# Kernel tuning notes

Hardware: AMD Instinct MI355X
Metric: run time of the kernel (lower is better)

The kernel has to match this reference:

```python
import jax, jax.numpy as jnp
import numpy as np

# Kernel codes matching style 'L;O2;P2;Y2,1,1;R0.5;W1,1'
KERNEL_CODES = ['L', 'O', 'P', 'Y', 'R', 'W']
SM_TEMP = 1.0


def _norm_sq(q, k):
    # q: [n,l,h,e], k: [n,s,h,e] -> [n,h,l,s]
    q2 = jnp.einsum('nlhe,nlhe->nhl', q, q)[..., None]        # [n,h,l,1]
    k2 = jnp.einsum('nshe,nshe->nhs', k, k)[:, :, None, :]     # [n,h,1,s]
    qk = jnp.einsum('nlhe,nshe->nhls', q, k)
    return q2 + k2 - 2.0 * qk


def _kernel(code, q, k):
    if code == 'L':
        return jnp.einsum('nlhe,nshe->nhls', q, k)
    if code == 'O':  # -log(1 + ns^(p/2)), p=2
        return -jnp.log1p(_norm_sq(q, k))
    if code == 'P':  # -(ns)^(p/2), p=2
        return -_norm_sq(q, k)
    if code == 'Y':  # (alpha*<q,k> + c)^p, p=2, alpha=1, c=1
        d = jnp.einsum('nlhe,nshe->nhls', q, k)
        return (d + 1.0) ** 2
    if code == 'R':  # exp(-gamma*ns), gamma=0.5
        return jnp.exp(-0.5 * _norm_sq(q, k))
    if code == 'W':  # cos(ns/a)*exp(-ns/b), a=b=1
        ns = _norm_sq(q, k)
        return jnp.cos(ns) * jnp.exp(-ns)
    raise ValueError(code)


def setup_inputs() -> dict:
    key = jax.random.key(0)
    k1, k2, k3, k4 = jax.random.split(key, 4)
    N, L, S, H, E, K = 2, 1024, 1024, 8, 64, 6
    return {
        'query': jax.random.normal(k1, (N, L, H, E), dtype=jnp.float32),
        'key': jax.random.normal(k2, (N, S, H, E), dtype=jnp.float32),
        'attn_mask_add': jnp.zeros((N, L, S), dtype=jnp.float32),
        'key_lengths_add': jnp.zeros((N, S), dtype=jnp.float32),
        'M': jax.random.uniform(k3, (H, E, K), dtype=jnp.float32),
        'C': jax.random.uniform(k4, (K, H, E, E), dtype=jnp.float32),
    }


def reference(query, key, attn_mask_add, key_lengths_add, M, C):
    # mixture weights pi: [n,l,h,k]
    pi = jax.nn.softmax(jnp.einsum('nlhe,hek->nlhk', query, M), axis=-1)
    out = None
    for c, code in enumerate(KERNEL_CODES):
        # htilde = tanh(query @ C[c]): [n,l,h,e]
        htilde = jnp.tanh(jnp.einsum('nlhe,hef->nlhf', query, C[c]))
        qk = _kernel(code, htilde, key)                    # [n,h,l,s]
        qk = qk + attn_mask_add[:, None] + key_lengths_add[:, None, None, :]
        sm = jax.nn.softmax(SM_TEMP * qk, axis=-1)
        w = jnp.transpose(pi[..., c], (0, 2, 1))[..., None]  # [n,h,l,1]
        term = sm * w
        out = term if out is None else out + term
    return out
```

## Files before the change

kernel.cpp:

```cpp
#include <hip/hip_runtime.h>
#include <hip/hip_bf16.h>
#include <math.h>

#define N_  2
#define H_  8
#define G_  16
#define L_  1024
#define S_  1024
#define E_  64
#define NC_ 6

typedef __attribute__((ext_vector_type(4))) float floatx4;
typedef __attribute__((ext_vector_type(8))) short short8;

#define MFMA16 __builtin_amdgcn_mfma_f32_16x16x32_bf16

#define AHAT_OFF   0
#define AHAT_BYTES (NC_*G_*L_*128*2)
#define KHAT_OFF   (AHAT_OFF + AHAT_BYTES)
#define KHAT_BYTES (G_*S_*128*2)
#define PI_OFF     (KHAT_OFF + KHAT_BYTES)
#define PI_BYTES   (NC_*G_*L_*4)
#define HSQ_OFF    (PI_OFF + PI_BYTES)
#define HSQ_BYTES  (NC_*G_*L_*4)
#define KSQ_OFF    (HSQ_OFF + HSQ_BYTES)
#define KSQ_BYTES  (G_*S_*4)

__device__ __forceinline__ float ftanh(float x) {
  return 1.0f - 2.0f * __builtin_amdgcn_rcpf(__expf(2.0f*x) + 1.0f);
}

__global__ __launch_bounds__(256) void k_htilde(
    const float* __restrict__ q, const float* __restrict__ C,
    __hip_bfloat16* __restrict__ Ahat, float* __restrict__ hsq) {
  extern __shared__ char smraw[];
  float* qs = (float*)smraw;
  float* Cs = qs + 128*68;

  const int lch = blockIdx.x, c = blockIdx.y, g = blockIdx.z;
  const int n = g >> 3, h = g & 7;
  const int l0 = lch * 128;
  const int t = threadIdx.x;

  for (int u = t; u < 2048; u += 256) {
    int row = u >> 4, seg = u & 15;
    *(float4*)(qs + row*68 + seg*4) =
      *(const float4*)(q + (((size_t)(n*L_ + l0 + row))*H_ + h)*E_ + seg*4);
  }
  for (int u = t; u < 1024; u += 256) {
    int e = u >> 4, seg = u & 15;
    *(float4*)(Cs + e*68 + seg*4) =
      *(const float4*)(C + (((size_t)(c*8 + h))*64 + e)*64 + seg*4);
  }
  __syncthreads();

  const int rg = t >> 3, fg = t & 7;
  float acc[4][8];
  #pragma unroll
  for (int i = 0; i < 4; i++)
    #pragma unroll
    for (int j = 0; j < 8; j++) acc[i][j] = 0.0f;

  #pragma unroll 4
  for (int e0 = 0; e0 < 64; e0 += 4) {
    float4 q4[4];
    #pragma unroll
    for (int i = 0; i < 4; i++)
      q4[i] = *(const float4*)(qs + (rg*4 + i)*68 + e0);
    #pragma unroll
    for (int ee = 0; ee < 4; ee++) {
      float4 ca = *(const float4*)(Cs + (e0+ee)*68 + fg*8);
      float4 cb = *(const float4*)(Cs + (e0+ee)*68 + fg*8 + 4);
      float c8[8] = {ca.x, ca.y, ca.z, ca.w, cb.x, cb.y, cb.z, cb.w};
      #pragma unroll
      for (int i = 0; i < 4; i++) {
        float qv = (ee == 0) ? q4[i].x : (ee == 1) ? q4[i].y
                 : (ee == 2) ? q4[i].z : q4[i].w;
        #pragma unroll
        for (int j = 0; j < 8; j++) acc[i][j] = fmaf(qv, c8[j], acc[i][j]);
      }
    }
  }

  #pragma unroll
  for (int i = 0; i < 4; i++) {
    int l = l0 + rg*4 + i;
    size_t rowb = (((size_t)(c*G_ + g))*L_ + l) * 128;
    float ss = 0.0f;
    short8 hi8, lo8;
    #pragma unroll
    for (int j = 0; j < 8; j++) {
      float hv = ftanh(acc[i][j]);
      ss += hv*hv;
      __hip_bfloat16 hi = __float2bfloat16(hv);
      __hip_bfloat16 lo = __float2bfloat16(hv - __bfloat162float(hi));
      short hs, ls;
      __builtin_memcpy(&hs, &hi, 2);
      __builtin_memcpy(&ls, &lo, 2);
      hi8[j] = hs; lo8[j] = ls;
    }
    *(short8*)((char*)Ahat + (rowb + fg*8)*2)      = hi8;
    *(short8*)((char*)Ahat + (rowb + 64 + fg*8)*2) = lo8;
    ss += __shfl_xor(ss, 1); ss += __shfl_xor(ss, 2); ss += __shfl_xor(ss, 4);
    if (fg == 0) hsq[((size_t)(c*G_ + g))*L_ + l] = ss;
  }
}

__global__ __launch_bounds__(256) void k_pi(
    const float* __restrict__ q, const float* __restrict__ M,
    float* __restrict__ pi_t) {
  __shared__ float Ms[384];
  const int g = blockIdx.x >> 2, lch = blockIdx.x & 3;
  const int n = g >> 3, h = g & 7;
  const int t = threadIdx.x;
  const int l = lch*256 + t;
  for (int u = t; u < 384; u += 256) Ms[u] = M[h*384 + u];
  __syncthreads();
  const float* qrow = q + (((size_t)(n*L_ + l))*H_ + h)*E_;
  float p[6] = {0.f, 0.f, 0.f, 0.f, 0.f, 0.f};
  #pragma unroll 8
  for (int e = 0; e < 64; e++) {
    float qv = qrow[e];
    #pragma unroll
    for (int k = 0; k < 6; k++) p[k] = fmaf(qv, Ms[e*6 + k], p[k]);
  }
  float mx = p[0];
  #pragma unroll
  for (int k = 1; k < 6; k++) mx = fmaxf(mx, p[k]);
  float den = 0.f;
  #pragma unroll
  for (int k = 0; k < 6; k++) den += __expf(p[k] - mx);
  float rden = __builtin_amdgcn_rcpf(den);
  #pragma unroll
  for (int k = 0; k < 6; k++)
    pi_t[((size_t)(k*G_ + g))*L_ + l] = __expf(p[k] - mx) * rden;
}

__global__ __launch_bounds__(256) void k_key(
    const float* __restrict__ key, __hip_bfloat16* __restrict__ Khat,
    float* __restrict__ ksq) {
  int t = threadIdx.x; int wv = t >> 6; int lane = t & 63;
  int r = blockIdx.x*4 + wv;
  int g = r >> 10; int s = r & 1023; int n = g >> 3; int h = g & 7;
  float v = key[(((size_t)(n*S_ + s))*H_ + h)*E_ + lane];
  __hip_bfloat16 hi = __float2bfloat16(v);
  __hip_bfloat16 lo = __float2bfloat16(v - __bfloat162float(hi));
  size_t base = ((size_t)g*S_ + s)*128;
  Khat[base + lane]      = hi;
  Khat[base + 64 + lane] = lo;
  float sq = v*v;
  #pragma unroll
  for (int off = 32; off; off >>= 1) sq += __shfl_xor(sq, off);
  if (lane == 0) ksq[(size_t)g*S_ + s] = sq;
}

#define LDS_K     0
#define LDS_KSQ   17408
#define LDS_KLEN  17664
#define LDS_ZRED  24576
#define LDS_MRED  26112
#define LDS_CST   27648
#define LDS_HSQ   28416
#define LDS_PI    28800
#define LDS_TOTAL 29184

__global__ __launch_bounds__(256, 2) void k_main(
    const __hip_bfloat16* __restrict__ Ahat, const __hip_bfloat16* __restrict__ Khat,
    const float* __restrict__ hsq, const float* __restrict__ ksq,
    const float* __restrict__ mask, const float* __restrict__ klen,
    const float* __restrict__ pi_t, float* __restrict__ out) {
  extern __shared__ char smraw[];
  char*   A6     = smraw;
  char*   K_lds  = smraw + LDS_K;
  float*  ksq_t  = (float*)(smraw + LDS_KSQ);
  float*  klen_t = (float*)(smraw + LDS_KLEN);
  float*  zred   = (float*)(smraw + LDS_ZRED);
  float*  mred   = (float*)(smraw + LDS_MRED);
  float2* cst    = (float2*)(smraw + LDS_CST);
  float*  hsq_s  = (float*)(smraw + LDS_HSQ);
  float*  pi_s   = (float*)(smraw + LDS_PI);

  const int l0 = blockIdx.x * 16; const int g = blockIdx.y; const int n = g >> 3;
  const int t = threadIdx.x; const int w = t >> 6; const int lane = t & 63;
  const int quad = lane >> 4; const int lc = lane & 15;

  #pragma unroll
  for (int rep = 0; rep < 6; rep++) {
    int u = t + rep*256; int cc = u >> 8; int rem = u & 255;
    int row = rem >> 4; int seg = rem & 15;
    *(int4*)(A6 + cc*4096 + row*256 + seg*16) =
      *(const int4*)((const char*)Ahat + (((size_t)(cc*G_+g))*L_ + l0 + row)*256 + seg*16);
  }
  if (t < 96) {
    size_t idx = ((size_t)((t >> 4)*G_ + g))*L_ + l0 + (t & 15);
    hsq_s[t] = hsq[idx];
    pi_s[t]  = pi_t[idx];
  }
  __syncthreads();

  short8 a6f[6][4];
  #pragma unroll
  for (int cc = 0; cc < 6; cc++)
    #pragma unroll
    for (int kt = 0; kt < 4; kt++)
      a6f[cc][kt] = *(const short8*)(A6 + cc*4096 + lc*256 + kt*64 + quad*16);

  float h1p[4], nh2[4], h4h[4], nh5[4];
  #pragma unroll
  for (int i = 0; i < 4; i++) {
    int r = quad*4 + i;
    h1p[i] = 1.0f + hsq_s[1*16 + r];
    nh2[i] = 64.0f - hsq_s[2*16 + r];
    h4h[i] = -0.5f * hsq_s[4*16 + r];
    nh5[i] = -hsq_s[5*16 + r];
  }

  float Zc[4][4], zp[4], m3[4], z3[4];
  #pragma unroll
  for (int i = 0; i < 4; i++) {
    #pragma unroll
    for (int c = 0; c < 4; c++) Zc[c][i] = 0.0f;
    zp[i] = 0.0f; m3[i] = -INFINITY; z3[i] = 0.0f;
  }

  #pragma unroll 1
  for (int st = 0; st < 16; st++) {
    int s0 = st*64;
    __syncthreads();
    #pragma unroll
    for (int rep = 0; rep < 4; rep++) {
      int u = t + rep*256; int row = u >> 4, seg = u & 15;
      *(int4*)(K_lds + row*272 + seg*16) =
        *(const int4*)((const char*)Khat + (((size_t)g)*S_ + s0 + row)*256 + seg*16);
    }
    if (t < 64) { ksq_t[t] = ksq[(size_t)g*S_ + s0 + t]; klen_t[t] = klen[(size_t)n*S_ + s0 + t]; }
    int scol = s0 + w*16 + lc;
    float mk[4];
    #pragma unroll
    for (int i = 0; i < 4; i++)
      mk[i] = mask[((size_t)(n*L_ + l0 + quad*4 + i))*S_ + scol];
    __syncthreads();
    short8 bfr[4];
    #pragma unroll
    for (int kt = 0; kt < 4; kt++)
      bfr[kt] = *(const short8*)(K_lds + (w*16 + lc)*272 + kt*64 + quad*16);
    float kq  = ksq_t[w*16 + lc];
    float klv = klen_t[w*16 + lc];
    float mv[4], Ev[4], oc[4], pc[4], rc[4], wc[4];
    #pragma unroll
    for (int i = 0; i < 4; i++) {
      mv[i] = mk[i] + klv;
      Ev[i] = __expf(mv[i]);
      oc[i] = h1p[i] + kq;
      pc[i] = nh2[i] - kq + mv[i];
      rc[i] = fmaf(-0.5f, kq, h4h[i]);
      wc[i] = nh5[i] - kq;
    }
    #pragma unroll
    for (int c = 0; c < 6; c++) {
      floatx4 a = {0.f, 0.f, 0.f, 0.f};
      a = MFMA16(a6f[c][0], bfr[0], a, 0,0,0);
      a = MFMA16(a6f[c][1], bfr[1], a, 0,0,0);
      a = MFMA16(a6f[c][0], bfr[2], a, 0,0,0);
      a = MFMA16(a6f[c][1], bfr[3], a, 0,0,0);
      a = MFMA16(a6f[c][2], bfr[0], a, 0,0,0);
      a = MFMA16(a6f[c][3], bfr[1], a, 0,0,0);
      #pragma unroll
      for (int i = 0; i < 4; i++) {
        float d = a[i];
        if (c == 0) {
          Zc[0][i] = fmaf(Ev[i], __expf(d), Zc[0][i]);
        } else if (c == 1) {
          Zc[1][i] = fmaf(Ev[i], __builtin_amdgcn_rcpf(fmaf(-2.f, d, oc[i])), Zc[1][i]);
        } else if (c == 2) {
          zp[i] += __expf(fmaf(2.f, d, pc[i]));
        } else if (c == 3) {
          float tt = d + 1.f;
          float x  = fmaf(tt, tt, mv[i]);
          float mn = fmaxf(m3[i], x);
          float e  = __expf(fminf(m3[i], x) - mn);
          z3[i] = (x > m3[i]) ? fmaf(z3[i], e, 1.0f) : (z3[i] + e);
          m3[i] = mn;
        } else if (c == 4) {
          Zc[2][i] = fmaf(Ev[i], __expf(__expf(d + rc[i])), Zc[2][i]);
        } else {
          float a5 = fmaf(2.f, d, wc[i]);
          Zc[3][i] = fmaf(Ev[i], __expf(__cosf(a5) * __expf(a5)), Zc[3][i]);
        }
      }
    }
  }

  #pragma unroll
  for (int off = 1; off < 16; off <<= 1) {
    #pragma unroll
    for (int c = 0; c < 4; c++)
      #pragma unroll
      for (int i = 0; i < 4; i++) Zc[c][i] += __shfl_xor(Zc[c][i], off);
    #pragma unroll
    for (int i = 0; i < 4; i++) {
      zp[i] += __shfl_xor(zp[i], off);
      float mo = __shfl_xor(m3[i], off);
      float zo = __shfl_xor(z3[i], off);
      float mn = fmaxf(m3[i], mo);
      float e  = __expf(fminf(m3[i], mo) - mn);
      z3[i] = (mo > m3[i]) ? fmaf(z3[i], e, zo) : fmaf(zo, e, z3[i]);
      m3[i] = mn;
    }
  }
  if (lc == 0) {
    static const int cmap[4] = {0, 1, 4, 5};
    #pragma unroll
    for (int c = 0; c < 4; c++)
      #pragma unroll
      for (int i = 0; i < 4; i++) {
        zred[w*96 + cmap[c]*16 + quad*4 + i] = Zc[c][i];
        mred[w*96 + cmap[c]*16 + quad*4 + i] = 0.f;
      }
    #pragma unroll
    for (int i = 0; i < 4; i++) {
      zred[w*96 + 2*16 + quad*4 + i] = zp[i];
      mred[w*96 + 2*16 + quad*4 + i] = 0.f;
      zred[w*96 + 3*16 + quad*4 + i] = z3[i];
      mred[w*96 + 3*16 + quad*4 + i] = m3[i];
    }
  }
  __syncthreads();
  if (t < 96) {
    int c = t >> 4;
    float z = zred[t], m = mred[t];
    if (c == 3) {
      #pragma unroll
      for (int w2 = 1; w2 < 4; w2++) {
        float mo = mred[w2*96 + t], zo = zred[w2*96 + t];
        float mn = fmaxf(m, mo);
        float e  = __expf(fminf(m, mo) - mn);
        z = (mo > m) ? fmaf(z, e, zo) : fmaf(zo, e, z);
        m = mn;
      }
    } else {
      #pragma unroll
      for (int w2 = 1; w2 < 4; w2++) z += zred[w2*96 + t];
    }
    cst[t] = make_float2(pi_s[t] / z, m);
  }
  __syncthreads();

  float ac[6][4], m3f[4];
  #pragma unroll
  for (int c = 0; c < 6; c++)
    #pragma unroll
    for (int i = 0; i < 4; i++) {
      float2 v = cst[c*16 + quad*4 + i];
      ac[c][i] = v.x;
      if (c == 3) m3f[i] = v.y;
    }

  #pragma unroll 1
  for (int st = 0; st < 16; st++) {
    int s0 = st*64;
    __syncthreads();
    #pragma unroll
    for (int rep = 0; rep < 4; rep++) {
      int u = t + rep*256; int row = u >> 4, seg = u & 15;
      *(int4*)(K_lds + row*272 + seg*16) =
        *(const int4*)((const char*)Khat + (((size_t)g)*S_ + s0 + row)*256 + seg*16);
    }
    if (t < 64) { ksq_t[t] = ksq[(size_t)g*S_ + s0 + t]; klen_t[t] = klen[(size_t)n*S_ + s0 + t]; }
    int scol = s0 + w*16 + lc;
    float mk[4];
    #pragma unroll
    for (int i = 0; i < 4; i++)
      mk[i] = mask[((size_t)(n*L_ + l0 + quad*4 + i))*S_ + scol];
    __syncthreads();
    short8 bfr[4];
    #pragma unroll
    for (int kt = 0; kt < 4; kt++)
      bfr[kt] = *(const short8*)(K_lds + (w*16 + lc)*272 + kt*64 + quad*16);
    float kq  = ksq_t[w*16 + lc];
    float klv = klen_t[w*16 + lc];
    float mv[4], Ev[4], oc[4], pc[4], rc[4], wc[4];
    #pragma unroll
    for (int i = 0; i < 4; i++) {
      mv[i] = mk[i] + klv;
      Ev[i] = __expf(mv[i]);
      oc[i] = h1p[i] + kq;
      pc[i] = nh2[i] - kq + mv[i];
      rc[i] = fmaf(-0.5f, kq, h4h[i]);
      wc[i] = nh5[i] - kq;
    }
    float Sacc[4] = {0.f, 0.f, 0.f, 0.f};
    float G[4]    = {0.f, 0.f, 0.f, 0.f};
    #pragma unroll
    for (int c = 0; c < 6; c++) {
      floatx4 a = {0.f, 0.f, 0.f, 0.f};
      a = MFMA16(a6f[c][0], bfr[0], a, 0,0,0);
      a = MFMA16(a6f[c][1], bfr[1], a, 0,0,0);
      a = MFMA16(a6f[c][0], bfr[2], a, 0,0,0);
      a = MFMA16(a6f[c][1], bfr[3], a, 0,0,0);
      a = MFMA16(a6f[c][2], bfr[0], a, 0,0,0);
      a = MFMA16(a6f[c][3], bfr[1], a, 0,0,0);
      #pragma unroll
      for (int i = 0; i < 4; i++) {
        float d = a[i];
        if (c == 0) {
          Sacc[i] = fmaf(ac[0][i], __expf(d), Sacc[i]);
        } else if (c == 1) {
          Sacc[i] = fmaf(ac[1][i], __builtin_amdgcn_rcpf(fmaf(-2.f, d, oc[i])), Sacc[i]);
        } else if (c == 2) {
          G[i] = fmaf(ac[2][i], __expf(fmaf(2.f, d, pc[i])), G[i]);
        } else if (c == 3) {
          float tt = d + 1.f;
          float x  = fmaf(tt, tt, mv[i]);
          G[i] = fmaf(ac[3][i], __expf(x - m3f[i]), G[i]);
        } else if (c == 4) {
          Sacc[i] = fmaf(ac[4][i], __expf(__expf(d + rc[i])), Sacc[i]);
        } else {
          float a5 = fmaf(2.f, d, wc[i]);
          Sacc[i] = fmaf(ac[5][i], __expf(__cosf(a5) * __expf(a5)), Sacc[i]);
        }
      }
    }
    #pragma unroll
    for (int i = 0; i < 4; i++)
      out[(((size_t)g)*L_ + l0 + quad*4 + i)*S_ + scol] = fmaf(Ev[i], Sacc[i], G[i]);
  }
}

extern "C" void kernel_launch(void* const* d_in, const int* in_sizes, int n_in,
                              void* d_out, int out_size, void* d_ws, size_t ws_size,
                              hipStream_t stream) {
  (void)in_sizes; (void)n_in; (void)out_size; (void)ws_size;
  const float* q    = (const float*)d_in[0];
  const float* key  = (const float*)d_in[1];
  const float* mask = (const float*)d_in[2];
  const float* klen = (const float*)d_in[3];
  const float* M    = (const float*)d_in[4];
  const float* C    = (const float*)d_in[5];
  char* ws = (char*)d_ws;
  __hip_bfloat16* Ahat = (__hip_bfloat16*)(ws + AHAT_OFF);
  __hip_bfloat16* Khat = (__hip_bfloat16*)(ws + KHAT_OFF);
  float* pi_t    = (float*)(ws + PI_OFF);
  float* hsq     = (float*)(ws + HSQ_OFF);
  float* ksq     = (float*)(ws + KSQ_OFF);
  float* out = (float*)d_out;

  k_htilde<<<dim3(8, 6, 16), 256, 52224, stream>>>(q, C, Ahat, hsq);
  k_key<<<4096, 256, 0, stream>>>(key, Khat, ksq);
  k_pi<<<64, 256, 0, stream>>>(q, M, pi_t);
  k_main<<<dim3(64, 16), 256, LDS_TOTAL, stream>>>(Ahat, Khat, hsq, ksq, mask, klen,
                                                   pi_t, out);
}
```

Baseline: 224.5 us.

## Load MFMA operands directly from global memory, dropping LDS staging and barriers

The kernel no longer stages the A6 query fragments, the K tiles, ksq, klen, hsq and pi through LDS. Each lane now reads its MFMA operand fragments and per-column scalars straight from global memory, which removes both per-iteration __syncthreads in the two S loops and shrinks LDS to the reduction buffers only. The aim is to cut barrier stalls and LDS traffic and to allow more resident blocks. The cost is that each wave reads its own K slice as strided 16-byte global loads, relying on L1/L2 for reuse, and that latency is exposed without prefetching.

```diff
diff --git a/kernel.cpp b/kernel.cpp
--- a/kernel.cpp
+++ b/kernel.cpp
@@ -154,15 +154,10 @@
   if (lane == 0) ksq[(size_t)g*S_ + s] = sq;
 }
 
-#define LDS_K     0
-#define LDS_KSQ   17408
-#define LDS_KLEN  17664
-#define LDS_ZRED  24576
-#define LDS_MRED  26112
-#define LDS_CST   27648
-#define LDS_HSQ   28416
-#define LDS_PI    28800
-#define LDS_TOTAL 29184
+#define LDS_ZRED  0
+#define LDS_MRED  1536
+#define LDS_CST   3072
+#define LDS_TOTAL 3840
 
 __global__ __launch_bounds__(256, 2) void k_main(
     const __hip_bfloat16* __restrict__ Ahat, const __hip_bfloat16* __restrict__ Khat,
@@ -170,49 +165,30 @@
     const float* __restrict__ mask, const float* __restrict__ klen,
     const float* __restrict__ pi_t, float* __restrict__ out) {
   extern __shared__ char smraw[];
-  char*   A6     = smraw;
-  char*   K_lds  = smraw + LDS_K;
-  float*  ksq_t  = (float*)(smraw + LDS_KSQ);
-  float*  klen_t = (float*)(smraw + LDS_KLEN);
   float*  zred   = (float*)(smraw + LDS_ZRED);
   float*  mred   = (float*)(smraw + LDS_MRED);
   float2* cst    = (float2*)(smraw + LDS_CST);
-  float*  hsq_s  = (float*)(smraw + LDS_HSQ);
-  float*  pi_s   = (float*)(smraw + LDS_PI);
 
   const int l0 = blockIdx.x * 16; const int g = blockIdx.y; const int n = g >> 3;
   const int t = threadIdx.x; const int w = t >> 6; const int lane = t & 63;
   const int quad = lane >> 4; const int lc = lane & 15;
 
-  #pragma unroll
-  for (int rep = 0; rep < 6; rep++) {
-    int u = t + rep*256; int cc = u >> 8; int rem = u & 255;
-    int row = rem >> 4; int seg = rem & 15;
-    *(int4*)(A6 + cc*4096 + row*256 + seg*16) =
-      *(const int4*)((const char*)Ahat + (((size_t)(cc*G_+g))*L_ + l0 + row)*256 + seg*16);
-  }
-  if (t < 96) {
-    size_t idx = ((size_t)((t >> 4)*G_ + g))*L_ + l0 + (t & 15);
-    hsq_s[t] = hsq[idx];
-    pi_s[t]  = pi_t[idx];
-  }
-  __syncthreads();
-
   short8 a6f[6][4];
   #pragma unroll
   for (int cc = 0; cc < 6; cc++)
     #pragma unroll
     for (int kt = 0; kt < 4; kt++)
-      a6f[cc][kt] = *(const short8*)(A6 + cc*4096 + lc*256 + kt*64 + quad*16);
+      a6f[cc][kt] = *(const short8*)((const char*)Ahat +
+          (((size_t)(cc*G_ + g))*L_ + l0 + lc)*256 + kt*64 + quad*16);
 
   float h1p[4], nh2[4], h4h[4], nh5[4];
   #pragma unroll
   for (int i = 0; i < 4; i++) {
     int r = quad*4 + i;
-    h1p[i] = 1.0f + hsq_s[1*16 + r];
-    nh2[i] = 64.0f - hsq_s[2*16 + r];
-    h4h[i] = -0.5f * hsq_s[4*16 + r];
-    nh5[i] = -hsq_s[5*16 + r];
+    h1p[i] = 1.0f + hsq[((size_t)(1*G_ + g))*L_ + l0 + r];
+    nh2[i] = 64.0f - hsq[((size_t)(2*G_ + g))*L_ + l0 + r];
+    h4h[i] = -0.5f * hsq[((size_t)(4*G_ + g))*L_ + l0 + r];
+    nh5[i] = -hsq[((size_t)(5*G_ + g))*L_ + l0 + r];
   }
 
   float Zc[4][4], zp[4], m3[4], z3[4];
@@ -226,26 +202,18 @@
   #pragma unroll 1
   for (int st = 0; st < 16; st++) {
     int s0 = st*64;
-    __syncthreads();
-    #pragma unroll
-    for (int rep = 0; rep < 4; rep++) {
-      int u = t + rep*256; int row = u >> 4, seg = u & 15;
-      *(int4*)(K_lds + row*272 + seg*16) =
-        *(const int4*)((const char*)Khat + (((size_t)g)*S_ + s0 + row)*256 + seg*16);
-    }
-    if (t < 64) { ksq_t[t] = ksq[(size_t)g*S_ + s0 + t]; klen_t[t] = klen[(size_t)n*S_ + s0 + t]; }
     int scol = s0 + w*16 + lc;
+    short8 bfr[4];
+    #pragma unroll
+    for (int kt = 0; kt < 4; kt++)
+      bfr[kt] = *(const short8*)((const char*)Khat +
+          (((size_t)g)*S_ + scol)*256 + kt*64 + quad*16);
+    float kq  = ksq[(size_t)g*S_ + scol];
+    float klv = klen[(size_t)n*S_ + scol];
     float mk[4];
     #pragma unroll
     for (int i = 0; i < 4; i++)
       mk[i] = mask[((size_t)(n*L_ + l0 + quad*4 + i))*S_ + scol];
-    __syncthreads();
-    short8 bfr[4];
-    #pragma unroll
-    for (int kt = 0; kt < 4; kt++)
-      bfr[kt] = *(const short8*)(K_lds + (w*16 + lc)*272 + kt*64 + quad*16);
-    float kq  = ksq_t[w*16 + lc];
-    float klv = klen_t[w*16 + lc];
     float mv[4], Ev[4], oc[4], pc[4], rc[4], wc[4];
     #pragma unroll
     for (int i = 0; i < 4; i++) {
@@ -342,7 +310,8 @@
       #pragma unroll
       for (int w2 = 1; w2 < 4; w2++) z += zred[w2*96 + t];
     }
-    cst[t] = make_float2(pi_s[t] / z, m);
+    float piv = pi_t[((size_t)((t >> 4)*G_ + g))*L_ + l0 + (t & 15)];
+    cst[t] = make_float2(piv / z, m);
   }
   __syncthreads();
 
@@ -359,26 +328,18 @@
   #pragma unroll 1
   for (int st = 0; st < 16; st++) {
     int s0 = st*64;
-    __syncthreads();
-    #pragma unroll
-    for (int rep = 0; rep < 4; rep++) {
-      int u = t + rep*256; int row = u >> 4, seg = u & 15;
-      *(int4*)(K_lds + row*272 + seg*16) =
-        *(const int4*)((const char*)Khat + (((size_t)g)*S_ + s0 + row)*256 + seg*16);
-    }
-    if (t < 64) { ksq_t[t] = ksq[(size_t)g*S_ + s0 + t]; klen_t[t] = klen[(size_t)n*S_ + s0 + t]; }
     int scol = s0 + w*16 + lc;
+    short8 bfr[4];
+    #pragma unroll
+    for (int kt = 0; kt < 4; kt++)
+      bfr[kt] = *(const short8*)((const char*)Khat +
+          (((size_t)g)*S_ + scol)*256 + kt*64 + quad*16);
+    float kq  = ksq[(size_t)g*S_ + scol];
+    float klv = klen[(size_t)n*S_ + scol];
     float mk[4];
     #pragma unroll
     for (int i = 0; i < 4; i++)
       mk[i] = mask[((size_t)(n*L_ + l0 + quad*4 + i))*S_ + scol];
-    __syncthreads();
-    short8 bfr[4];
-    #pragma unroll
-    for (int kt = 0; kt < 4; kt++)
-      bfr[kt] = *(const short8*)(K_lds + (w*16 + lc)*272 + kt*64 + quad*16);
-    float kq  = ksq_t[w*16 + lc];
-    float klv = klen_t[w*16 + lc];
     float mv[4], Ev[4], oc[4], pc[4], rc[4], wc[4];
     #pragma unroll
     for (int i = 0; i < 4; i++) {
```

Result: no change. 226.7 us (+1.0%).
